# Kernel tuning notes

Measured on AMD Instinct MI355X. Metric: run time of the kernel, lower is better.

The kernel has to match this reference:

```python
import jax, jax.numpy as jnp
import numpy as np

D_MODEL = 512
NUM_HEADS = 8


def setup_inputs() -> dict:
    key = jax.random.key(0)
    ks = jax.random.split(key, 12)
    B, S, D = 2, 4096, D_MODEL
    scale = 1.0 / np.sqrt(D)
    inp = {
        "q": jax.random.normal(ks[0], (B, S, D), jnp.float32),
        "k": jax.random.normal(ks[1], (B, S, D), jnp.float32),
        "v": jax.random.normal(ks[2], (B, S, D), jnp.float32),
        "w_q": jax.random.normal(ks[3], (D, D), jnp.float32) * scale,
        "b_q": jax.random.normal(ks[4], (D,), jnp.float32) * scale,
        "w_k": jax.random.normal(ks[5], (D, D), jnp.float32) * scale,
        "b_k": jax.random.normal(ks[6], (D,), jnp.float32) * scale,
        "w_v": jax.random.normal(ks[7], (D, D), jnp.float32) * scale,
        "b_v": jax.random.normal(ks[8], (D,), jnp.float32) * scale,
        "w_o": jax.random.normal(ks[9], (D, D), jnp.float32) * scale,
        "b_o": jax.random.normal(ks[10], (D,), jnp.float32) * scale,
    }
    return inp


def _split_heads(x, h):
    b, s, d = x.shape
    return x.reshape(b, s, h, d // h).transpose(0, 2, 1, 3)  # [B,H,S,dk]


def reference(q, k, v, w_q, b_q, w_k, b_k, w_v, b_v, w_o, b_o):
    h = NUM_HEADS
    # Linear projections (torch Linear: x @ W.T + b)
    qh = _split_heads(q @ w_q.T + b_q, h)
    kh = _split_heads(k @ w_k.T + b_k, h)
    vh = _split_heads(v @ w_v.T + b_v, h)
    d_k = kh.shape[-1]
    scores = jnp.einsum("bhsd,bhtd->bhst", qh, kh) / jnp.sqrt(jnp.float32(d_k))
    attn = jax.nn.softmax(scores, axis=-1)  # [B,H,S,S] - materialized, as in source
    out = jnp.einsum("bhst,bhtd->bhsd", attn, vh)
    b, _, s, dk = out.shape
    out = out.transpose(0, 2, 1, 3).reshape(b, s, h * dk)
    return out @ w_o.T + b_o
```

## Files before the change

### kernel.cpp

```cpp
#include <hip/hip_runtime.h>
#include <hip/hip_bf16.h>

#define D_MODEL 512
#define NHEAD   8
#define DK      64
#define SEQ     4096
#define BATCH   2
#define NTOK    (BATCH * SEQ)

typedef __bf16 bf16;
typedef __bf16 bf16x2 __attribute__((ext_vector_type(2)));
typedef __bf16 bf16x4 __attribute__((ext_vector_type(4)));
typedef __bf16 bf16x8 __attribute__((ext_vector_type(8)));
typedef float  f32x4  __attribute__((ext_vector_type(4)));
typedef float  f32x16 __attribute__((ext_vector_type(16)));
typedef unsigned u32x4 __attribute__((ext_vector_type(4)));

#define MFMA16(a, b, c) __builtin_amdgcn_mfma_f32_16x16x32_bf16((a), (b), (c), 0, 0, 0)
#define MFMA32(a, b, c) __builtin_amdgcn_mfma_f32_32x32x16_bf16((a), (b), (c), 0, 0, 0)

#define QSCALE 0.18033688f

__device__ __forceinline__ unsigned pkbf16(float a, float b) {
    bf16x2 t = {(bf16)a, (bf16)b};
    return __builtin_bit_cast(unsigned, t);
}

__global__ __launch_bounds__(256) void cvt_w(
    const float* __restrict__ wq, const float* __restrict__ wk,
    const float* __restrict__ wv, const float* __restrict__ wo,
    bf16* __restrict__ Wb)
{
    int i = blockIdx.x * 256 + threadIdx.x;
    int m = i >> 16;
    int g = i & 65535;
    const float* src = (m == 0) ? wq : (m == 1) ? wk : (m == 2) ? wv : wo;
    float4 x = *(const float4*)(src + (size_t)g * 4);
    bf16x4 y = {(bf16)x.x, (bf16)x.y, (bf16)x.z, (bf16)x.w};
    *(bf16x4*)(Wb + (size_t)m * D_MODEL * D_MODEL + (size_t)g * 4) = y;
}

__global__ __launch_bounds__(256, 3) void proj_qkv(
    const float* __restrict__ q, const float* __restrict__ k, const float* __restrict__ v,
    const bf16* __restrict__ Wb,
    const float* __restrict__ bq, const float* __restrict__ bk, const float* __restrict__ bv,
    bf16* __restrict__ Qh, bf16* __restrict__ Kh, bf16* __restrict__ Vt)
{
    const int p = blockIdx.z;
    const float* X    = (p == 0) ? q  : (p == 1) ? k  : v;
    const bf16*  W    = Wb + (size_t)p * D_MODEL * D_MODEL;
    const float* bias = (p == 0) ? bq : (p == 1) ? bk : bv;

    __shared__ union __align__(16) {
        struct { bf16 As[128][72]; bf16 Bs[128][72]; } g;
        bf16 T[128][136];
    } sm;

    const int m0   = blockIdx.x * 128;
    const int n0   = blockIdx.y * 128;
    const int tid  = threadIdx.x;
    const int lane = tid & 63;
    const int wave = tid >> 6;
    const int low4 = lane & 15;
    const int quad = lane >> 4;
    const int wm   = wave >> 1;
    const int wn   = wave & 1;

    int srow[8], sc4[8];
    for (int it = 0; it < 8; ++it) {
        int idx = tid + it * 256;
        srow[it] = idx >> 4;
        sc4[it]  = (idx & 15) * 4;
    }
    int br[4], bc[4];
    for (int it = 0; it < 4; ++it) {
        int idx = tid + it * 256;
        br[it] = idx >> 3;
        bc[it] = (idx & 7) * 8;
    }

    float4 gA[8];
    bf16x8 gB[4];
    for (int it = 0; it < 8; ++it)
        gA[it] = *(const float4*)(X + (size_t)(m0 + srow[it]) * D_MODEL + sc4[it]);
    for (int it = 0; it < 4; ++it)
        gB[it] = *(const bf16x8*)(W + (size_t)(n0 + br[it]) * D_MODEL + bc[it]);

    f32x4 acc[4][4];
    for (int i = 0; i < 4; ++i)
        for (int j = 0; j < 4; ++j)
            acc[i][j] = f32x4{0.f, 0.f, 0.f, 0.f};

    for (int k0 = 0; k0 < D_MODEL; k0 += 64) {
        __syncthreads();
        for (int it = 0; it < 8; ++it) {
            bf16x4 wa = {(bf16)gA[it].x, (bf16)gA[it].y, (bf16)gA[it].z, (bf16)gA[it].w};
            *(bf16x4*)&sm.g.As[srow[it]][sc4[it]] = wa;
        }
        for (int it = 0; it < 4; ++it)
            *(bf16x8*)&sm.g.Bs[br[it]][bc[it]] = gB[it];
        __syncthreads();

        if (k0 + 64 < D_MODEL) {
            for (int it = 0; it < 8; ++it)
                gA[it] = *(const float4*)(X + (size_t)(m0 + srow[it]) * D_MODEL + k0 + 64 + sc4[it]);
            for (int it = 0; it < 4; ++it)
                gB[it] = *(const bf16x8*)(W + (size_t)(n0 + br[it]) * D_MODEL + k0 + 64 + bc[it]);
        }

        for (int ks = 0; ks < 2; ++ks) {
            bf16x8 a[4], b[4];
            for (int i = 0; i < 4; ++i)
                a[i] = *(const bf16x8*)&sm.g.As[wm * 64 + i * 16 + low4][ks * 32 + quad * 8];
            for (int j = 0; j < 4; ++j)
                b[j] = *(const bf16x8*)&sm.g.Bs[wn * 64 + j * 16 + low4][ks * 32 + quad * 8];
            for (int i = 0; i < 4; ++i)
                for (int j = 0; j < 4; ++j)
                    acc[i][j] = MFMA16(a[i], b[j], acc[i][j]);
        }
    }

    if (p < 2) {
        bf16* Out = (p == 0) ? Qh : Kh;
        const float sc = (p == 0) ? QSCALE : 1.0f;
        for (int j = 0; j < 4; ++j) {
            int col = n0 + wn * 64 + j * 16 + low4;
            float bcol = bias[col];
            for (int i = 0; i < 4; ++i)
                for (int r = 0; r < 4; ++r) {
                    int row = m0 + wm * 64 + i * 16 + quad * 4 + r;
                    Out[(size_t)row * D_MODEL + col] = (bf16)((acc[i][j][r] + bcol) * sc);
                }
        }
    } else {
        __syncthreads();
        for (int j = 0; j < 4; ++j) {
            int col = n0 + wn * 64 + j * 16 + low4;
            float bcol = bias[col];
            for (int i = 0; i < 4; ++i)
                for (int r = 0; r < 4; ++r)
                    sm.T[wn * 64 + j * 16 + low4][wm * 64 + i * 16 + quad * 4 + r] =
                        (bf16)(acc[i][j][r] + bcol);
        }
        __syncthreads();
        const int bb = m0 >> 12;
        const int s0 = (m0 & 4095);
        for (int it = 0; it < 8; ++it) {
            int cc = it * 16 + (tid >> 4);
            int ml = (tid & 15) * 8;
            int col = n0 + cc;
            int hh = col >> 6, dd = col & 63;
            *(bf16x8*)&Vt[(((size_t)(bb * NHEAD + hh) * DK + dd) << 12) + s0 + ml] =
                *(const bf16x8*)&sm.T[cc][ml];
        }
    }
}

__global__ __launch_bounds__(512, 4) void attn(
    const bf16* __restrict__ Qh, const bf16* __restrict__ Kh,
    const bf16* __restrict__ Vt, bf16* __restrict__ O)
{
    __shared__ union __align__(16) {
        struct { bf16 K[2][128 * 64]; bf16 V[2][64 * 128]; } s;
        float Obuf[4][32][68];
    } sm;
    __shared__ float Lbuf[4][32];

    const int q0   = blockIdx.x * 128;
    const int bh   = blockIdx.y;
    const int b    = bh >> 3, h = bh & 7;
    const int tid  = threadIdx.x;
    const int lane = tid & 63;
    const int wave = tid >> 6;
    const int qg   = wave >> 1;
    const int kg   = wave & 1;
    const int m32  = lane & 31;
    const int hl   = lane >> 5;
    const int rb   = m32 & 7;

    const bf16* Kbase = Kh + (size_t)b * SEQ * D_MODEL + h * DK;
    const bf16* Vbase = Vt + (size_t)bh * DK * SEQ;

    const bf16* Qrow = Qh + (size_t)(b * SEQ + q0 + qg * 32 + m32) * D_MODEL + h * DK;
    bf16x8 qf[4];
    for (int ks = 0; ks < 4; ++ks)
        qf[ks] = *(const bf16x8*)(Qrow + ks * 16 + hl * 8);

    float l = 0.f;
    f32x16 acc[2];
    for (int i = 0; i < 16; ++i) { acc[0][i] = 0.f; acc[1][i] = 0.f; }

    int kr[2], kc[2], vr[2], vc[2], kso[2], vso[2];
    for (int it = 0; it < 2; ++it) {
        int c = tid + it * 512;
        kr[it] = c >> 3;  kc[it] = (c & 7) * 8;
        vr[it] = c >> 4;  vc[it] = (c & 15) * 8;
        kso[it] = kr[it] * 64  + (((c & 7)  ^ (kr[it] & 7)) << 3);
        vso[it] = vr[it] * 128 + (((c & 15) ^ (vr[it] & 7)) << 3);
    }

    bf16x8 gk[2], gv[2];
    for (int it = 0; it < 2; ++it) {
        gk[it] = *(const bf16x8*)(Kbase + (size_t)kr[it] * D_MODEL + kc[it]);
        gv[it] = *(const bf16x8*)(Vbase + (size_t)vr[it] * SEQ + vc[it]);
    }
    for (int it = 0; it < 2; ++it) {
        *(bf16x8*)&sm.s.K[0][kso[it]] = gk[it];
        *(bf16x8*)&sm.s.V[0][vso[it]] = gv[it];
    }

    for (int t0 = 0; t0 < SEQ; t0 += 128) {
        const int cur = (t0 >> 7) & 1;
        const bf16* Kc = sm.s.K[cur];
        const bf16* Vc = sm.s.V[cur];

        const bool pf_next = (t0 + 128 < SEQ);
        if (pf_next) {
            for (int it = 0; it < 2; ++it) {
                gk[it] = *(const bf16x8*)(Kbase + (size_t)(t0 + 128 + kr[it]) * D_MODEL + kc[it]);
                gv[it] = *(const bf16x8*)(Vbase + (size_t)vr[it] * SEQ + t0 + 128 + vc[it]);
            }
        }

        __syncthreads();

        for (int mt = 0; mt < 2; ++mt) {
            f32x16 sc;
            for (int i = 0; i < 16; ++i) sc[i] = 0.f;
            const int krow = kg * 64 + mt * 32 + m32;
            __builtin_amdgcn_s_setprio(1);
            for (int ks = 0; ks < 4; ++ks) {
                bf16x8 kf = *(const bf16x8*)&Kc[krow * 64 + (((ks * 2 + hl) ^ rb) << 3)];
                sc = MFMA32(kf, qf[ks], sc);
            }
            __builtin_amdgcn_s_setprio(0);

            u32x4 pa, pb;
            {
                float p0 = __builtin_amdgcn_exp2f(sc[0]);
                float p1 = __builtin_amdgcn_exp2f(sc[1]);
                float p2 = __builtin_amdgcn_exp2f(sc[2]);
                float p3 = __builtin_amdgcn_exp2f(sc[3]);
                l += (p0 + p1) + (p2 + p3);
                unsigned y0 = pkbf16(p0, p1), y1 = pkbf16(p2, p3);
                p0 = __builtin_amdgcn_exp2f(sc[4]);
                p1 = __builtin_amdgcn_exp2f(sc[5]);
                p2 = __builtin_amdgcn_exp2f(sc[6]);
                p3 = __builtin_amdgcn_exp2f(sc[7]);
                l += (p0 + p1) + (p2 + p3);
                unsigned y2 = pkbf16(p0, p1), y3 = pkbf16(p2, p3);
                auto s0 = __builtin_amdgcn_permlane32_swap(y0, y2, false, false);
                auto s1 = __builtin_amdgcn_permlane32_swap(y1, y3, false, false);
                pa[0] = s0[0]; pa[2] = s0[1]; pa[1] = s1[0]; pa[3] = s1[1];

                p0 = __builtin_amdgcn_exp2f(sc[8]);
                p1 = __builtin_amdgcn_exp2f(sc[9]);
                p2 = __builtin_amdgcn_exp2f(sc[10]);
                p3 = __builtin_amdgcn_exp2f(sc[11]);
                l += (p0 + p1) + (p2 + p3);
                y0 = pkbf16(p0, p1); y1 = pkbf16(p2, p3);
                p0 = __builtin_amdgcn_exp2f(sc[12]);
                p1 = __builtin_amdgcn_exp2f(sc[13]);
                p2 = __builtin_amdgcn_exp2f(sc[14]);
                p3 = __builtin_amdgcn_exp2f(sc[15]);
                l += (p0 + p1) + (p2 + p3);
                y2 = pkbf16(p0, p1); y3 = pkbf16(p2, p3);
                auto s2 = __builtin_amdgcn_permlane32_swap(y0, y2, false, false);
                auto s3 = __builtin_amdgcn_permlane32_swap(y1, y3, false, false);
                pb[0] = s2[0]; pb[2] = s2[1]; pb[1] = s3[0]; pb[3] = s3[1];
            }
            bf16x8 pfa = __builtin_bit_cast(bf16x8, pa);
            bf16x8 pfb = __builtin_bit_cast(bf16x8, pb);

            __builtin_amdgcn_s_setprio(1);
            for (int nt = 0; nt < 2; ++nt) {
                const int vrow = nt * 32 + m32;
                bf16x8 va = *(const bf16x8*)&Vc[vrow * 128 + (((kg * 8 + (2 * mt) * 2 + hl) ^ rb) << 3)];
                acc[nt] = MFMA32(pfa, va, acc[nt]);
                bf16x8 vb = *(const bf16x8*)&Vc[vrow * 128 + (((kg * 8 + (2 * mt + 1) * 2 + hl) ^ rb) << 3)];
                acc[nt] = MFMA32(pfb, vb, acc[nt]);
            }
            __builtin_amdgcn_s_setprio(0);
        }

        if (pf_next) {
            bf16* Kn = sm.s.K[cur ^ 1];
            bf16* Vn = sm.s.V[cur ^ 1];
            for (int it = 0; it < 2; ++it) {
                *(bf16x8*)&Kn[kso[it]] = gk[it];
                *(bf16x8*)&Vn[vso[it]] = gv[it];
            }
        }
    }

    l += __shfl_xor(l, 32);
    __syncthreads();
    if (kg == 1) {
        for (int nt = 0; nt < 2; ++nt)
            for (int r = 0; r < 16; ++r) {
                int qq = (r & 3) + 8 * (r >> 2) + 4 * hl;
                sm.Obuf[qg][qq][nt * 32 + m32] = acc[nt][r];
            }
        if (hl == 0) Lbuf[qg][m32] = l;
    }
    __syncthreads();
    if (kg == 0) {
        float lt  = l + Lbuf[qg][m32];
        float inv = 1.0f / lt;
        for (int nt = 0; nt < 2; ++nt)
            for (int r = 0; r < 16; ++r) {
                int qq = (r & 3) + 8 * (r >> 2) + 4 * hl;
                float val = acc[nt][r] + sm.Obuf[qg][qq][nt * 32 + m32];
                float iv  = __shfl(inv, qq);
                O[(size_t)(b * SEQ + q0 + qg * 32 + qq) * D_MODEL + h * DK + nt * 32 + m32] =
                    (bf16)(val * iv);
            }
    }
}

__global__ __launch_bounds__(256, 4) void proj_out(
    const bf16* __restrict__ Oin, const bf16* __restrict__ Wo,
    const float* __restrict__ bo, float* __restrict__ out)
{
    __shared__ bf16 As[64][72];
    __shared__ bf16 Bs[64][72];

    const int m0   = blockIdx.x * 64;
    const int n0   = blockIdx.y * 64;
    const int tid  = threadIdx.x;
    const int lane = tid & 63;
    const int wave = tid >> 6;
    const int low4 = lane & 15;
    const int quad = lane >> 4;
    const int wm   = wave >> 1;
    const int wn   = wave & 1;

    int arow[2], ag[2];
    for (int it = 0; it < 2; ++it) {
        int idx = tid + it * 256;
        arow[it] = idx >> 3;
        ag[it]   = (idx & 7) * 8;
    }

    bf16x8 gA[2], gB[2];
    for (int it = 0; it < 2; ++it) {
        gA[it] = *(const bf16x8*)(Oin + (size_t)(m0 + arow[it]) * D_MODEL + ag[it]);
        gB[it] = *(const bf16x8*)(Wo + (size_t)(n0 + arow[it]) * D_MODEL + ag[it]);
    }

    f32x4 acc[2][2];
    for (int i = 0; i < 2; ++i)
        for (int j = 0; j < 2; ++j)
            acc[i][j] = f32x4{0.f, 0.f, 0.f, 0.f};

    for (int k0 = 0; k0 < D_MODEL; k0 += 64) {
        __syncthreads();
        for (int it = 0; it < 2; ++it) {
            *(bf16x8*)&As[arow[it]][ag[it]] = gA[it];
            *(bf16x8*)&Bs[arow[it]][ag[it]] = gB[it];
        }
        __syncthreads();

        if (k0 + 64 < D_MODEL) {
            for (int it = 0; it < 2; ++it) {
                gA[it] = *(const bf16x8*)(Oin + (size_t)(m0 + arow[it]) * D_MODEL + k0 + 64 + ag[it]);
                gB[it] = *(const bf16x8*)(Wo + (size_t)(n0 + arow[it]) * D_MODEL + k0 + 64 + ag[it]);
            }
        }

        for (int ks = 0; ks < 2; ++ks) {
            bf16x8 a[2], b[2];
            for (int i = 0; i < 2; ++i)
                a[i] = *(const bf16x8*)&As[wm * 32 + i * 16 + low4][ks * 32 + quad * 8];
            for (int j = 0; j < 2; ++j)
                b[j] = *(const bf16x8*)&Bs[wn * 32 + j * 16 + low4][ks * 32 + quad * 8];
            for (int i = 0; i < 2; ++i)
                for (int j = 0; j < 2; ++j)
                    acc[i][j] = MFMA16(a[i], b[j], acc[i][j]);
        }
    }

    for (int j = 0; j < 2; ++j) {
        int col = n0 + wn * 32 + j * 16 + low4;
        float bcol = bo[col];
        for (int i = 0; i < 2; ++i)
            for (int r = 0; r < 4; ++r) {
                int row = m0 + wm * 32 + i * 16 + quad * 4 + r;
                out[(size_t)row * D_MODEL + col] = acc[i][j][r] + bcol;
            }
    }
}

extern "C" void kernel_launch(void* const* d_in, const int* in_sizes, int n_in,
                              void* d_out, int out_size, void* d_ws, size_t ws_size,
                              hipStream_t stream)
{
    const float* q  = (const float*)d_in[0];
    const float* k  = (const float*)d_in[1];
    const float* v  = (const float*)d_in[2];
    const float* wq = (const float*)d_in[3];
    const float* bq = (const float*)d_in[4];
    const float* wk = (const float*)d_in[5];
    const float* bk = (const float*)d_in[6];
    const float* wv = (const float*)d_in[7];
    const float* bv = (const float*)d_in[8];
    const float* wo = (const float*)d_in[9];
    const float* bo = (const float*)d_in[10];

    const size_t NT = (size_t)NTOK * D_MODEL;
    bf16* Qh = (bf16*)d_ws;
    bf16* Kh = Qh + NT;
    bf16* Vt = Kh + NT;
    bf16* O  = Vt + NT;
    bf16* Wb = O + NT;

    cvt_w<<<1024, 256, 0, stream>>>(wq, wk, wv, wo, Wb);

    dim3 g1(NTOK / 128, D_MODEL / 128, 3);
    proj_qkv<<<g1, 256, 0, stream>>>(q, k, v, Wb, bq, bk, bv, Qh, Kh, Vt);

    dim3 g2(SEQ / 128, BATCH * NHEAD);
    attn<<<g2, 512, 0, stream>>>(Qh, Kh, Vt, O);

    dim3 g3(NTOK / 64, D_MODEL / 64);
    proj_out<<<g3, 256, 0, stream>>>(O, Wb + (size_t)3 * D_MODEL * D_MODEL, bo, (float*)d_out);
}
```

Before: 244.1 us.

## Replace swizzled double-buffered K/V tiles with padded single buffer

Drops the double-buffered, XOR-swizzled K/V shared tiles in favor of a single padded tile written at the top of each iteration between two barriers, with global prefetch into registers kept. Removes the setprio hints and relaxes launch bounds from 4 to 2 blocks per CU. This halves the LDS footprint and frees registers, trading away overlap of LDS writes with compute and adding an extra barrier per tile.

```diff
diff --git a/kernel.cpp b/kernel.cpp
--- a/kernel.cpp
+++ b/kernel.cpp
@@ -156,12 +156,12 @@
     }
 }
 
-__global__ __launch_bounds__(512, 4) void attn(
+__global__ __launch_bounds__(512, 2) void attn(
     const bf16* __restrict__ Qh, const bf16* __restrict__ Kh,
     const bf16* __restrict__ Vt, bf16* __restrict__ O)
 {
     __shared__ union __align__(16) {
-        struct { bf16 K[2][128 * 64]; bf16 V[2][64 * 128]; } s;
+        struct { bf16 Ks[128][72]; bf16 Vs[64][136]; } s;
         float Obuf[4][32][68];
     } sm;
     __shared__ float Lbuf[4][32];
@@ -176,7 +176,6 @@
     const int kg   = wave & 1;
     const int m32  = lane & 31;
     const int hl   = lane >> 5;
-    const int rb   = m32 & 7;
 
     const bf16* Kbase = Kh + (size_t)b * SEQ * D_MODEL + h * DK;
     const bf16* Vbase = Vt + (size_t)bh * DK * SEQ;
@@ -190,50 +189,40 @@
     f32x16 acc[2];
     for (int i = 0; i < 16; ++i) { acc[0][i] = 0.f; acc[1][i] = 0.f; }
 
-    int kr[2], kc[2], vr[2], vc[2], kso[2], vso[2];
+    int kr[2], kc[2], vr[2], vc[2];
     for (int it = 0; it < 2; ++it) {
         int c = tid + it * 512;
         kr[it] = c >> 3;  kc[it] = (c & 7) * 8;
         vr[it] = c >> 4;  vc[it] = (c & 15) * 8;
-        kso[it] = kr[it] * 64  + (((c & 7)  ^ (kr[it] & 7)) << 3);
-        vso[it] = vr[it] * 128 + (((c & 15) ^ (vr[it] & 7)) << 3);
-    }
-
+    }
     bf16x8 gk[2], gv[2];
     for (int it = 0; it < 2; ++it) {
         gk[it] = *(const bf16x8*)(Kbase + (size_t)kr[it] * D_MODEL + kc[it]);
         gv[it] = *(const bf16x8*)(Vbase + (size_t)vr[it] * SEQ + vc[it]);
     }
-    for (int it = 0; it < 2; ++it) {
-        *(bf16x8*)&sm.s.K[0][kso[it]] = gk[it];
-        *(bf16x8*)&sm.s.V[0][vso[it]] = gv[it];
-    }
 
     for (int t0 = 0; t0 < SEQ; t0 += 128) {
-        const int cur = (t0 >> 7) & 1;
-        const bf16* Kc = sm.s.K[cur];
-        const bf16* Vc = sm.s.V[cur];
-
-        const bool pf_next = (t0 + 128 < SEQ);
-        if (pf_next) {
+        __syncthreads();
+        for (int it = 0; it < 2; ++it) {
+            *(bf16x8*)&sm.s.Ks[kr[it]][kc[it]] = gk[it];
+            *(bf16x8*)&sm.s.Vs[vr[it]][vc[it]] = gv[it];
+        }
+        __syncthreads();
+
+        if (t0 + 128 < SEQ) {
             for (int it = 0; it < 2; ++it) {
                 gk[it] = *(const bf16x8*)(Kbase + (size_t)(t0 + 128 + kr[it]) * D_MODEL + kc[it]);
                 gv[it] = *(const bf16x8*)(Vbase + (size_t)vr[it] * SEQ + t0 + 128 + vc[it]);
             }
         }
 
-        __syncthreads();
-
         for (int mt = 0; mt < 2; ++mt) {
             f32x16 sc;
             for (int i = 0; i < 16; ++i) sc[i] = 0.f;
-            const int krow = kg * 64 + mt * 32 + m32;
-            __builtin_amdgcn_s_setprio(1);
             for (int ks = 0; ks < 4; ++ks) {
-                bf16x8 kf = *(const bf16x8*)&Kc[krow * 64 + (((ks * 2 + hl) ^ rb) << 3)];
+                bf16x8 kf = *(const bf16x8*)&sm.s.Ks[kg * 64 + mt * 32 + m32][ks * 16 + hl * 8];
                 sc = MFMA32(kf, qf[ks], sc);
             }
-            __builtin_amdgcn_s_setprio(0);
 
             u32x4 pa, pb;
             {
@@ -272,23 +261,11 @@
             bf16x8 pfa = __builtin_bit_cast(bf16x8, pa);
             bf16x8 pfb = __builtin_bit_cast(bf16x8, pb);
 
-            __builtin_amdgcn_s_setprio(1);
             for (int nt = 0; nt < 2; ++nt) {
-                const int vrow = nt * 32 + m32;
-                bf16x8 va = *(const bf16x8*)&Vc[vrow * 128 + (((kg * 8 + (2 * mt) * 2 + hl) ^ rb) << 3)];
+                bf16x8 va = *(const bf16x8*)&sm.s.Vs[nt * 32 + m32][kg * 64 + (2 * mt) * 16 + hl * 8];
                 acc[nt] = MFMA32(pfa, va, acc[nt]);
-                bf16x8 vb = *(const bf16x8*)&Vc[vrow * 128 + (((kg * 8 + (2 * mt + 1) * 2 + hl) ^ rb) << 3)];
+                bf16x8 vb = *(const bf16x8*)&sm.s.Vs[nt * 32 + m32][kg * 64 + (2 * mt + 1) * 16 + hl * 8];
                 acc[nt] = MFMA32(pfb, vb, acc[nt]);
-            }
-            __builtin_amdgcn_s_setprio(0);
-        }
-
-        if (pf_next) {
-            bf16* Kn = sm.s.K[cur ^ 1];
-            bf16* Vn = sm.s.V[cur ^ 1];
-            for (int it = 0; it < 2; ++it) {
-                *(bf16x8*)&Kn[kso[it]] = gk[it];
-                *(bf16x8*)&Vn[vso[it]] = gv[it];
             }
         }
     }
```

Measured after the change: 238.2 us. 2.4% less time.
